# Kernel optimization log

Measured on AMD Instinct MI355X. Metric: run time of the kernel, lower is better.

## Reference

```python
import jax, jax.numpy as jnp
import numpy as np

V = 128
L = 128
N = 4096

_ALPHA = "abcdefghijklmnopqrstuvwxyz"
TOKENS = (list("+-*/^()=") + [f"temp_{a}" for a in _ALPHA]
          + [str(d) for d in range(10)] + [f"w{i}" for i in range(84)])
assert len(TOKENS) == V
IDX = {t: i for i, t in enumerate(TOKENS)}
TEMPS = [f"temp_{a}" for a in _ALPHA]


def _build_mask_table() -> np.ndarray:
    """mask_table[p, v] = 0 if token v is illegal after prev-token p, else 1.
    Mirrors RuleFilter.single_filter's rho for every possible prev token."""
    M = np.ones((V, V), dtype=np.float32)

    def ban(prev_tokens, banned_tokens):
        cols = [IDX[t] for t in banned_tokens]
        for p in prev_tokens:
            M[IDX[p], cols] = 0.0

    ban(list("+-*/"), list("+-*/)="))          # prev is binary op
    ban(TEMPS, list("(="))                      # prev is temp_* variable
    ban(["="], list("+-*/=)") + TEMPS)         # prev is '='
    ban(["("], list("()+-*/="))                # prev is '('
    ban([")"], list("()") + TEMPS)             # prev is ')'
    ban(["^"], list("+-*/=)"))                 # prev is '^'
    return M


def setup_inputs() -> dict:
    key = jax.random.key(0)
    logits = jax.random.normal(key, (L, N, V), dtype=jnp.float32)
    mask_table = jnp.asarray(_build_mask_table())  # (V, V) rule lookup
    return {"logits": logits, "mask_table": mask_table}


def reference(logits, mask_table):
    """logits: (L, N, V); mask_table: (V, V). Sequential rule masking:
    logits[i] *= mask_table[argmax(filtered logits[i-1])]."""
    first = logits[0]  # row 0 is never filtered

    def step(carry, cur):
        # carry: previously *filtered* logits row (N, V)
        prev_idx = jnp.argmax(carry, axis=-1)          # (N,)
        new = cur * mask_table[prev_idx]               # gather + multiply
        return new, new

    _, rest = jax.lax.scan(step, first, logits[1:])
    return jnp.concatenate([first[None], rest], axis=0)
```

## Files before the change

kernel.cpp:

```cpp
#include <hip/hip_runtime.h>


constexpr int V = 128;
constexpr int L = 128;
constexpr int N = 4096;
constexpr int D  = 15;
constexpr int RD = 16;
constexpr unsigned ROWB = (unsigned)N * V * 4;

typedef __attribute__((ext_vector_type(2))) float f32x2;
typedef unsigned long long u64;

__device__ __forceinline__ float wave_max_dpp(float x) {
    int v = __float_as_int(x);
    const int ninf = __float_as_int(-__builtin_inff());
#define RF_STEP(ctrl)                                                          \
    {                                                                          \
        int s = __builtin_amdgcn_update_dpp(ninf, v, ctrl, 0xf, 0xf, false);   \
        v = __float_as_int(fmaxf(__int_as_float(v), __int_as_float(s)));       \
    }
    RF_STEP(0x111) RF_STEP(0x112) RF_STEP(0x114) RF_STEP(0x118)
    RF_STEP(0x142) RF_STEP(0x143)
#undef RF_STEP
    return __int_as_float(__builtin_amdgcn_readlane(v, 63));
}

__device__ __forceinline__ int wave_argmax(f32x2 f) {
    const float bv = wave_max_dpp(fmaxf(f.x, f.y));
    u64 b0 = __ballot(f.x == bv);
    u64 b1 = __ballot(f.y == bv);
    int i0 = __ffsll(b0), i1 = __ffsll(b1);
    int c0 = i0 ? (i0 - 1) * 2 : (1 << 30);
    int c1 = i1 ? (i1 - 1) * 2 + 1 : (1 << 30);
    return min(c0, c1);
}

__device__ __forceinline__ unsigned sel8(const unsigned* t, int j) {
    unsigned a0 = (j & 1) ? t[1] : t[0];
    unsigned a1 = (j & 1) ? t[3] : t[2];
    unsigned a2 = (j & 1) ? t[5] : t[4];
    unsigned a3 = (j & 1) ? t[7] : t[6];
    unsigned b0 = (j & 2) ? a1 : a0;
    unsigned b1 = (j & 2) ? a3 : a2;
    return (j & 4) ? b1 : b0;
}

__device__ __forceinline__ u64 uniform_u64(const void* p) {
    u64 x = (u64)p;
    unsigned lo = __builtin_amdgcn_readfirstlane((unsigned)x);
    unsigned hi = __builtin_amdgcn_readfirstlane((unsigned)(x >> 32));
    return ((u64)hi << 32) | lo;
}

template <bool PROD, int PH, int J>
struct Walk {
    static constexpr int  NW    = PROD ? ((PH == 2 && J > 0) ? (15 - J) : 15)
                                       : ((PH == 0) ? (15 + J)
                                          : ((PH == 2 && J > 0) ? (30 - J) : 30));
    static constexpr bool PF    = (PH != 2) || (J == 0);
    static constexpr bool FIRST = (PH == 0 && J == 0);
    static constexpr bool LAST  = (PH == 2 && J == 15);
    static constexpr int  rs    = J & 15;
    static constexpr int  ps    = (J + D) & 15;

    static __device__ __forceinline__ void run(f32x2* ring, const unsigned* tbl,
                                               int& prev, int irow, unsigned ibase,
                                               u64 lbase, u64 obase,
                                               volatile unsigned* flg, int lane) {
        if constexpr (PF) {
            unsigned voff = ibase + (unsigned)(J + D) * ROWB;
            asm volatile("global_load_dwordx2 %0, %1, %2"
                         : "=&v"(ring[ps])
                         : "v"(voff), "s"(lbase));
        }

        asm volatile("s_waitcnt vmcnt(%c1)" : "+v"(ring[rs]) : "i"(NW));

        f32x2 c = ring[rs];

        if constexpr (PROD) {
            f32x2 f;
            if constexpr (FIRST) {
                f = c;
            } else {
                unsigned word = sel8(tbl, prev >> 4);
                unsigned fb   = (word >> ((prev & 15) * 2)) & 3u;
                f.x = (fb & 1u) ? c.x : 0.0f;
                f.y = (fb & 2u) ? c.y : 0.0f;
            }
            if constexpr (!LAST) {
                prev = wave_argmax(f);
                if (lane == 0) flg[irow + J + 1] = 0x100u | (unsigned)prev;
            }
        } else {
            f32x2 f;
            if constexpr (FIRST) {
                f = c;
            } else {
                unsigned v;
                while ((v = flg[irow + J]) == 0u) {}
                int pv = (int)(v & 127u);
                unsigned word = sel8(tbl, pv >> 4);
                unsigned fb   = (word >> ((pv & 15) * 2)) & 3u;
                f.x = (fb & 1u) ? c.x : 0.0f;
                f.y = (fb & 2u) ? c.y : 0.0f;
            }
            ring[rs] = f;
            unsigned voff = ibase + (unsigned)J * ROWB;
            asm volatile("global_store_dwordx2 %0, %1, %2"
                         :: "v"(voff), "v"(ring[rs]), "s"(obase));
        }

        Walk<PROD, PH, J + 1>::run(ring, tbl, prev, irow, ibase, lbase, obase,
                                   flg, lane);
    }
};
template <bool PROD, int PH>
struct Walk<PROD, PH, 16> {
    static __device__ __forceinline__ void run(f32x2*, const unsigned*, int&,
                                               int, unsigned, u64, u64,
                                               volatile unsigned*, int) {}
};

template <bool PROD>
__device__ __forceinline__ void walk_all(f32x2* ring, const unsigned* tbl,
                                         u64 lbase, u64 obase,
                                         volatile unsigned* flg,
                                         int lane, unsigned laneoff) {
    int prev = 0;
    int irow = 0;
    unsigned ibase = laneoff;
    Walk<PROD, 0, 0>::run(ring, tbl, prev, irow, ibase, lbase, obase, flg, lane);
    irow = 16; ibase += 16u * ROWB;
#pragma unroll 1
    for (int m = 0; m < 6; ++m) {
        Walk<PROD, 1, 0>::run(ring, tbl, prev, irow, ibase, lbase, obase, flg, lane);
        irow += 16; ibase += 16u * ROWB;
    }
    Walk<PROD, 2, 0>::run(ring, tbl, prev, irow, ibase, lbase, obase, flg, lane);
}

__global__ __launch_bounds__(128, 8) void rule_filter_kernel(
    const float* __restrict__ logits,
    const float* __restrict__ mask_table,
    float* __restrict__ out)
{
    __shared__ unsigned flgs[132];

    const int h    = threadIdx.x >> 6;
    const int lane = threadIdx.x & 63;
    const int n    = blockIdx.x;

    const u64 lbase = uniform_u64(logits + (size_t)n * V);
    const u64 obase = uniform_u64(out    + (size_t)n * V);
    const unsigned laneoff = (unsigned)lane * 8;

    unsigned tbl[8];
#pragma unroll 1
    for (int j = 0; j < 8; ++j) {
        unsigned acc = 0;
#pragma unroll
        for (int r = 0; r < 16; ++r) {
            const int p = j * 16 + r;
            float2 mv = *(const float2*)(mask_table + (size_t)p * V + lane * 2);
            acc |= ((mv.x != 0.0f ? 1u : 0u) | (mv.y != 0.0f ? 2u : 0u)) << (2 * r);
        }
        tbl[j] = acc;
    }

    flgs[threadIdx.x] = 0;
    if (threadIdx.x < 4) flgs[128 + threadIdx.x] = 0;
    __syncthreads();
    asm volatile("s_waitcnt vmcnt(0)" ::: "memory");

    f32x2 ring[RD];
#pragma unroll
    for (int r = 0; r < D; ++r) {
        unsigned voff = (unsigned)r * ROWB + laneoff;
        asm volatile("global_load_dwordx2 %0, %1, %2"
                     : "=&v"(ring[r])
                     : "v"(voff), "s"(lbase));
    }

    volatile unsigned* flg = flgs;
    if (h == 0) walk_all<true >(ring, tbl, lbase, obase, flg, lane, laneoff);
    else        walk_all<false>(ring, tbl, lbase, obase, flg, lane, laneoff);

    asm volatile("s_waitcnt vmcnt(0)" ::: "memory");
}

extern "C" void kernel_launch(void* const* d_in, const int* in_sizes, int n_in,
                              void* d_out, int out_size, void* d_ws, size_t ws_size,
                              hipStream_t stream) {
    const float* logits     = (const float*)d_in[0];
    const float* mask_table = (const float*)d_in[1];
    float* out              = (float*)d_out;

    dim3 grid(N);
    dim3 block(128);
    rule_filter_kernel<<<grid, block, 0, stream>>>(logits, mask_table, out);
}
```

Measured before the change: 479.5 us.

## Load logits once per block and hand rows to argmax wave via LDS

Previously both waves of each block issued their own global loads for every logits row. Now only wave 0 streams rows from global memory: it copies each row into a four-slot LDS ring and raises a ready flag. Wave 1 reads the row from LDS, runs the sequential argmax chain, and publishes the previous-token index back through a second flag array. This halves global read traffic, at the cost of an extra LDS write/wait handshake that may sit on the latency-critical argmax dependency chain.

```diff
diff --git a/kernel.cpp b/kernel.cpp
--- a/kernel.cpp
+++ b/kernel.cpp
@@ -52,21 +52,22 @@
     return ((u64)hi << 32) | lo;
 }
 
-template <bool PROD, int PH, int J>
-struct Walk {
-    static constexpr int  NW    = PROD ? ((PH == 2 && J > 0) ? (15 - J) : 15)
-                                       : ((PH == 0) ? (15 + J)
-                                          : ((PH == 2 && J > 0) ? (30 - J) : 30));
+template <int PH, int J>
+struct CWalk {
+    static constexpr int  NW    = (PH == 0) ? (15 + J)
+                                 : ((PH == 2 && J > 0) ? (30 - J) : 30);
     static constexpr bool PF    = (PH != 2) || (J == 0);
     static constexpr bool FIRST = (PH == 0 && J == 0);
-    static constexpr bool LAST  = (PH == 2 && J == 15);
     static constexpr int  rs    = J & 15;
     static constexpr int  ps    = (J + D) & 15;
 
     static __device__ __forceinline__ void run(f32x2* ring, const unsigned* tbl,
-                                               int& prev, int irow, unsigned ibase,
+                                               int irow, unsigned ibase,
                                                u64 lbase, u64 obase,
-                                               volatile unsigned* flg, int lane) {
+                                               float* rowbuf,
+                                               volatile unsigned* flag_r,
+                                               volatile unsigned* flag_p,
+                                               int lane) {
         if constexpr (PF) {
             unsigned voff = ibase + (unsigned)(J + D) * ROWB;
             asm volatile("global_load_dwordx2 %0, %1, %2"
@@ -75,79 +76,53 @@
         }
 
         asm volatile("s_waitcnt vmcnt(%c1)" : "+v"(ring[rs]) : "i"(NW));
-
         f32x2 c = ring[rs];
 
-        if constexpr (PROD) {
-            f32x2 f;
-            if constexpr (FIRST) {
-                f = c;
-            } else {
-                unsigned word = sel8(tbl, prev >> 4);
-                unsigned fb   = (word >> ((prev & 15) * 2)) & 3u;
-                f.x = (fb & 1u) ? c.x : 0.0f;
-                f.y = (fb & 2u) ? c.y : 0.0f;
-            }
-            if constexpr (!LAST) {
-                prev = wave_argmax(f);
-                if (lane == 0) flg[irow + J + 1] = 0x100u | (unsigned)prev;
-            }
+        *(f32x2*)&rowbuf[((irow + J) & 3) * V + lane * 2] = c;
+        asm volatile("s_waitcnt lgkmcnt(0)" ::: "memory");
+        if (lane == 0) flag_r[irow + J] = 1u;
+
+        f32x2 f;
+        if constexpr (FIRST) {
+            f = c;
         } else {
-            f32x2 f;
-            if constexpr (FIRST) {
-                f = c;
-            } else {
-                unsigned v;
-                while ((v = flg[irow + J]) == 0u) {}
-                int pv = (int)(v & 127u);
-                unsigned word = sel8(tbl, pv >> 4);
-                unsigned fb   = (word >> ((pv & 15) * 2)) & 3u;
-                f.x = (fb & 1u) ? c.x : 0.0f;
-                f.y = (fb & 2u) ? c.y : 0.0f;
-            }
-            ring[rs] = f;
+            unsigned v;
+            while (((v = flag_p[irow + J]) & 0x100u) == 0u) {}
+            int pv = (int)(v & 127u);
+            unsigned word = sel8(tbl, pv >> 4);
+            unsigned fb   = (word >> ((pv & 15) * 2)) & 3u;
+            f.x = (fb & 1u) ? c.x : 0.0f;
+            f.y = (fb & 2u) ? c.y : 0.0f;
+        }
+        ring[rs] = f;
+        {
             unsigned voff = ibase + (unsigned)J * ROWB;
             asm volatile("global_store_dwordx2 %0, %1, %2"
                          :: "v"(voff), "v"(ring[rs]), "s"(obase));
         }
 
-        Walk<PROD, PH, J + 1>::run(ring, tbl, prev, irow, ibase, lbase, obase,
-                                   flg, lane);
+        CWalk<PH, J + 1>::run(ring, tbl, irow, ibase, lbase, obase, rowbuf,
+                              flag_r, flag_p, lane);
     }
 };
-template <bool PROD, int PH>
-struct Walk<PROD, PH, 16> {
-    static __device__ __forceinline__ void run(f32x2*, const unsigned*, int&,
-                                               int, unsigned, u64, u64,
+template <int PH>
+struct CWalk<PH, 16> {
+    static __device__ __forceinline__ void run(f32x2*, const unsigned*, int,
+                                               unsigned, u64, u64, float*,
+                                               volatile unsigned*,
                                                volatile unsigned*, int) {}
 };
-
-template <bool PROD>
-__device__ __forceinline__ void walk_all(f32x2* ring, const unsigned* tbl,
-                                         u64 lbase, u64 obase,
-                                         volatile unsigned* flg,
-                                         int lane, unsigned laneoff) {
-    int prev = 0;
-    int irow = 0;
-    unsigned ibase = laneoff;
-    Walk<PROD, 0, 0>::run(ring, tbl, prev, irow, ibase, lbase, obase, flg, lane);
-    irow = 16; ibase += 16u * ROWB;
-#pragma unroll 1
-    for (int m = 0; m < 6; ++m) {
-        Walk<PROD, 1, 0>::run(ring, tbl, prev, irow, ibase, lbase, obase, flg, lane);
-        irow += 16; ibase += 16u * ROWB;
-    }
-    Walk<PROD, 2, 0>::run(ring, tbl, prev, irow, ibase, lbase, obase, flg, lane);
-}
 
 __global__ __launch_bounds__(128, 8) void rule_filter_kernel(
     const float* __restrict__ logits,
     const float* __restrict__ mask_table,
     float* __restrict__ out)
 {
-    __shared__ unsigned flgs[132];
-
-    const int h    = threadIdx.x >> 6;
+    __shared__ float    rowbuf[4 * V];
+    __shared__ unsigned flagr[L];
+    __shared__ unsigned flagp[L];
+
+    const int w    = threadIdx.x >> 6;
     const int lane = threadIdx.x & 63;
     const int n    = blockIdx.x;
 
@@ -168,25 +143,56 @@
         tbl[j] = acc;
     }
 
-    flgs[threadIdx.x] = 0;
-    if (threadIdx.x < 4) flgs[128 + threadIdx.x] = 0;
+    flagr[threadIdx.x] = 0;
+    flagp[threadIdx.x] = 0;
     __syncthreads();
-    asm volatile("s_waitcnt vmcnt(0)" ::: "memory");
-
-    f32x2 ring[RD];
+
+    volatile unsigned* flag_r = flagr;
+    volatile unsigned* flag_p = flagp;
+
+    if (w == 0) {
+        f32x2 ring[RD];
 #pragma unroll
-    for (int r = 0; r < D; ++r) {
-        unsigned voff = (unsigned)r * ROWB + laneoff;
-        asm volatile("global_load_dwordx2 %0, %1, %2"
-                     : "=&v"(ring[r])
-                     : "v"(voff), "s"(lbase));
-    }
-
-    volatile unsigned* flg = flgs;
-    if (h == 0) walk_all<true >(ring, tbl, lbase, obase, flg, lane, laneoff);
-    else        walk_all<false>(ring, tbl, lbase, obase, flg, lane, laneoff);
-
-    asm volatile("s_waitcnt vmcnt(0)" ::: "memory");
+        for (int r = 0; r < D; ++r) {
+            unsigned voff = (unsigned)r * ROWB + laneoff;
+            asm volatile("global_load_dwordx2 %0, %1, %2"
+                         : "=&v"(ring[r])
+                         : "v"(voff), "s"(lbase));
+        }
+        int irow = 0;
+        unsigned ibase = laneoff;
+        CWalk<0, 0>::run(ring, tbl, irow, ibase, lbase, obase, rowbuf,
+                         flag_r, flag_p, lane);
+        irow = 16; ibase += 16u * ROWB;
+#pragma unroll 1
+        for (int m = 0; m < 6; ++m) {
+            CWalk<1, 0>::run(ring, tbl, irow, ibase, lbase, obase, rowbuf,
+                             flag_r, flag_p, lane);
+            irow += 16; ibase += 16u * ROWB;
+        }
+        CWalk<2, 0>::run(ring, tbl, irow, ibase, lbase, obase, rowbuf,
+                         flag_r, flag_p, lane);
+        asm volatile("s_waitcnt vmcnt(0)" ::: "memory");
+    } else {
+        int prev = 0;
+#pragma unroll 1
+        for (int i = 0; i < L - 1; ++i) {
+            while (flag_r[i] == 0u) {}
+            asm volatile("" ::: "memory");
+            f32x2 c = *(f32x2*)&rowbuf[(i & 3) * V + lane * 2];
+            f32x2 f;
+            if (i == 0) {
+                f = c;
+            } else {
+                unsigned word = sel8(tbl, prev >> 4);
+                unsigned fb   = (word >> ((prev & 15) * 2)) & 3u;
+                f.x = (fb & 1u) ? c.x : 0.0f;
+                f.y = (fb & 2u) ? c.y : 0.0f;
+            }
+            prev = wave_argmax(f);
+            if (lane == 0) flag_p[i + 1] = 0x100u | (unsigned)prev;
+        }
+    }
 }
 
 extern "C" void kernel_launch(void* const* d_in, const int* in_sizes, int n_in,
```

Result: slower. 505.1 us (+5.3%).
